# Kernel optimization log

Hardware: AMD Instinct MI355X
Metric: run time of the kernel (lower is better)

Reference implementation:

```python
import jax, jax.numpy as jnp
import numpy as np

STIM_KER_LEN = 50  # length of causal stimulus kernel
K_BASIS = 2        # number of exponential basis functions in history kernel


def setup_inputs() -> dict:
    key = jax.random.key(0)
    T, NTR = 8192, 1024
    k0, k1, k2 = jax.random.split(key, 3)
    t = jnp.arange(T, dtype=jnp.float32)                    # uniform grid, dt = 1.0
    stim = jax.random.normal(k0, (T,), jnp.float32)
    rand = jax.random.uniform(k1, (T, NTR), jnp.float32)    # per-step uniforms (torch.rand in loop)
    # learned parameters
    bias = jnp.array([-4.0], jnp.float32)                   # nn.Parameter bias
    k_stim = jax.random.normal(k2, (STIM_KER_LEN,), jnp.float32) * 0.1  # stim kernel weights
    hist_w = jnp.array([-5.0, 1.0], jnp.float32)            # exponential basis coefficients
    hist_tau = jnp.array([5.0, 20.0], jnp.float32)          # exponential basis time constants
    return dict(t=t, stim=stim, rand=rand, bias=bias, k_stim=k_stim,
                hist_w=hist_w, hist_tau=hist_tau)


def reference(t, stim, rand, bias, k_stim, hist_w, hist_tau):
    dt = t[1] - t[0]
    T = t.shape[0]
    ntr = rand.shape[1]
    # stim_kernel(stim, dt): causal convolution scaled by dt, then shift_tensor(..., 1, fill=0)
    stim_conv = jnp.convolve(stim, k_stim)[:T] * dt                       # (T,)
    stim_conv = jnp.concatenate([jnp.zeros((1,), stim.dtype), stim_conv[:-1]])
    # history kernel: ker(s) = sum_k hist_w[k] * exp(-s / hist_tau[k]), evaluated from 0
    # one step after each spike -> linear recurrence on per-basis state s (K, ntr).
    decay = jnp.exp(-dt / hist_tau)                                        # (K,)

    def step(s, inp):
        sc_j, r_j = inp                       # scalar, (ntr,)
        hist_j = jnp.sum(s, axis=0)           # (ntr,) == hist_conv[j]
        loglam_j = bias[0] + sc_j + hist_j    # (ntr,)
        p_spk = 1.0 - jnp.exp(-jnp.exp(loglam_j) * dt)
        spk_j = p_spk > r_j                   # (ntr,) bool
        s_new = decay[:, None] * s + hist_w[:, None] * spk_j.astype(s.dtype)
        return s_new, (loglam_j, spk_j)

    s0 = jnp.zeros((hist_w.shape[0], ntr), jnp.float32)
    _, (log_lam, mask_spikes) = jax.lax.scan(step, s0, (stim_conv, rand))
    return log_lam, mask_spikes
```

## Files before the change

kernel.cpp:

```cpp
#include <hip/hip_runtime.h>
#include <math.h>

#define T_LEN 8192
#define NTRIALS 1024
#define TN ((size_t)T_LEN * NTRIALS)
#define KLEN 50
#define CHUNK 64
#define NCHUNK (T_LEN / CHUNK)
#define FARW 256
#define NEARW 256
#define WARM (FARW + NEARW)
#define PF 32
#define BAND 1e-4f

__global__ __launch_bounds__(256) void prep_fused_kernel(
    const float* __restrict__ t, const float* __restrict__ stim,
    const float* __restrict__ bias, const float* __restrict__ k_stim,
    const float* __restrict__ hist_w, const float* __restrict__ hist_tau,
    const float* __restrict__ rnd, double* __restrict__ dparams,
    double* __restrict__ basc, float* __restrict__ bascf,
    float* __restrict__ thr32) {
  const int j = blockIdx.x;
  const int tid = threadIdx.x;
  const double dt = (double)t[1] - (double)t[0];

  double acc = 0.0;
  if (j > 0) {
    int n = j - 1;
    int mmax = n < (KLEN - 1) ? n : (KLEN - 1);
    for (int m = 0; m <= mmax; ++m)
      acc += (double)k_stim[m] * (double)stim[n - m];
  }
  double b64 = (double)bias[0] + (j > 0 ? dt * acc : 0.0);
  float bf = (float)b64;

  if (tid == 0) {
    basc[j] = b64;
    bascf[j] = bf;
    if (j == 0) {
      dparams[0] = exp(-dt / (double)hist_tau[0]);
      dparams[1] = exp(-dt / (double)hist_tau[1]);
      dparams[2] = (double)hist_w[0];
      dparams[3] = (double)hist_w[1];
      dparams[4] = dt;
    }
  }

  const float dtf = (float)dt;
  size_t m = (size_t)j * NTRIALS + (size_t)tid * 4;
  float4 r4 = *reinterpret_cast<const float4*>(rnd + m);
  float4 o;
  o.x = logf(-log1pf(-r4.x) / dtf) - bf;
  o.y = logf(-log1pf(-r4.y) / dtf) - bf;
  o.z = logf(-log1pf(-r4.z) / dtf) - bf;
  o.w = logf(-log1pf(-r4.w) / dtf) - bf;
  *reinterpret_cast<float4*>(thr32 + m) = o;
}

__device__ __noinline__ bool decide64(const float* __restrict__ rnd,
                                      const double* __restrict__ basc,
                                      double dt, int j, int i, double h) {
  double r = (double)rnd[(size_t)j * NTRIALS + i];
  double t = log(-log1p(-r) / dt) - basc[j];
  return h > t;
}

__global__ __launch_bounds__(64, 1) void spec_scan4_kernel(
    const float* __restrict__ thr, const float* __restrict__ rnd,
    const double* __restrict__ basc, const float* __restrict__ bascf,
    const double* __restrict__ dparams, float* __restrict__ out) {
  const int tid = threadIdx.x;
  const int tb  = blockIdx.x & 15;
  const int c   = blockIdx.x >> 4;
  const int i   = tb * 64 + tid;
  const double d0 = dparams[0], d1 = dparams[1];
  const double w0 = dparams[2], w1 = dparams[3];
  const double dt = dparams[4];
  const float d0f = (float)d0, d1f = (float)d1;
  const float w0f = (float)w0, w1f = (float)w1;

  const int jstart = c * CHUNK;
  const int nw    = jstart < WARM ? jstart : WARM;
  const int jw    = jstart - nw;
  const int nearn = nw < NEARW ? nw : NEARW;
  const int farn  = nw - nearn;
  const int j1    = jw + farn;

  const float* __restrict__ p = thr + i;
  float bufA[PF], bufB[PF];
#pragma unroll
  for (int k = 0; k < PF; ++k) bufA[k] = p[(size_t)(jw + k) * NTRIALS];
  __builtin_amdgcn_sched_barrier(0);

  float a0 = 0.0f, a1 = 0.0f;
  for (int q = 0; q < farn; q += 2 * PF) {
    const int j0 = jw + q;
#pragma unroll
    for (int k = 0; k < PF; ++k) bufB[k] = p[(size_t)(j0 + PF + k) * NTRIALS];
    __builtin_amdgcn_sched_barrier(0);
#pragma unroll
    for (int k = 0; k < PF; ++k) {
      float h = a0 + a1;
      bool s = h > bufA[k];
      a0 = fmaf(d0f, a0, s ? w0f : 0.0f);
      a1 = fmaf(d1f, a1, s ? w1f : 0.0f);
    }
    __builtin_amdgcn_sched_barrier(0);
#pragma unroll
    for (int k = 0; k < PF; ++k) bufA[k] = p[(size_t)(j0 + 2 * PF + k) * NTRIALS];
    __builtin_amdgcn_sched_barrier(0);
#pragma unroll
    for (int k = 0; k < PF; ++k) {
      float h = a0 + a1;
      bool s = h > bufB[k];
      a0 = fmaf(d0f, a0, s ? w0f : 0.0f);
      a1 = fmaf(d1f, a1, s ? w1f : 0.0f);
    }
    __builtin_amdgcn_sched_barrier(0);
  }

  double s0 = (double)a0, s1 = (double)a1;
  for (int q = 0; q < nearn; q += 2 * PF) {
    const int j0 = j1 + q;
#pragma unroll
    for (int k = 0; k < PF; ++k) bufB[k] = p[(size_t)(j0 + PF + k) * NTRIALS];
    __builtin_amdgcn_sched_barrier(0);
#pragma unroll
    for (int k = 0; k < PF; ++k) {
      double h = s0 + s1;
      float d = (float)h - bufA[k];
      bool s = d > 0.0f;
      if (__builtin_expect(fabsf(d) < BAND, 0))
        s = decide64(rnd, basc, dt, j0 + k, i, h);
      s0 = fma(d0, s0, s ? w0 : 0.0);
      s1 = fma(d1, s1, s ? w1 : 0.0);
    }
    __builtin_amdgcn_sched_barrier(0);
#pragma unroll
    for (int k = 0; k < PF; ++k) bufA[k] = p[(size_t)(j0 + 2 * PF + k) * NTRIALS];
    __builtin_amdgcn_sched_barrier(0);
#pragma unroll
    for (int k = 0; k < PF; ++k) {
      double h = s0 + s1;
      float d = (float)h - bufB[k];
      bool s = d > 0.0f;
      if (__builtin_expect(fabsf(d) < BAND, 0))
        s = decide64(rnd, basc, dt, j0 + PF + k, i, h);
      s0 = fma(d0, s0, s ? w0 : 0.0);
      s1 = fma(d1, s1, s ? w1 : 0.0);
    }
    __builtin_amdgcn_sched_barrier(0);
  }

  float* __restrict__ po_ll = out + (size_t)jstart * NTRIALS + i;
  float* __restrict__ po_mk = po_ll + TN;
#pragma unroll
  for (int k = 0; k < PF; ++k) bufB[k] = p[(size_t)(jstart + PF + k) * NTRIALS];
  __builtin_amdgcn_sched_barrier(0);
#pragma unroll
  for (int k = 0; k < PF; ++k) {
    double h = s0 + s1;
    float d = (float)h - bufA[k];
    bool s = d > 0.0f;
    if (__builtin_expect(fabsf(d) < BAND, 0))
      s = decide64(rnd, basc, dt, jstart + k, i, h);
    __builtin_nontemporal_store((float)h + bascf[jstart + k], po_ll + (size_t)k * NTRIALS);
    __builtin_nontemporal_store(s ? 1.0f : 0.0f, po_mk + (size_t)k * NTRIALS);
    s0 = fma(d0, s0, s ? w0 : 0.0);
    s1 = fma(d1, s1, s ? w1 : 0.0);
  }
  __builtin_amdgcn_sched_barrier(0);
#pragma unroll
  for (int k = 0; k < PF; ++k) {
    double h = s0 + s1;
    float d = (float)h - bufB[k];
    bool s = d > 0.0f;
    if (__builtin_expect(fabsf(d) < BAND, 0))
      s = decide64(rnd, basc, dt, jstart + PF + k, i, h);
    __builtin_nontemporal_store((float)h + bascf[jstart + PF + k], po_ll + (size_t)(PF + k) * NTRIALS);
    __builtin_nontemporal_store(s ? 1.0f : 0.0f, po_mk + (size_t)(PF + k) * NTRIALS);
    s0 = fma(d0, s0, s ? w0 : 0.0);
    s1 = fma(d1, s1, s ? w1 : 0.0);
  }
}

__global__ __launch_bounds__(64, 1) void glm_scan_inline_kernel(
    const float* __restrict__ rnd, const float* __restrict__ t,
    const float* __restrict__ stim, const float* __restrict__ bias,
    const float* __restrict__ k_stim, const float* __restrict__ hist_w,
    const float* __restrict__ hist_tau, float* __restrict__ out) {
  const int i = blockIdx.x * 64 + threadIdx.x;
  const double dt = (double)t[1] - (double)t[0];
  const double d0 = exp(-dt / (double)hist_tau[0]);
  const double d1 = exp(-dt / (double)hist_tau[1]);
  const double w0 = (double)hist_w[0], w1 = (double)hist_w[1];
  double s0 = 0.0, s1 = 0.0;
  float* __restrict__ out_ll = out;
  float* __restrict__ out_mk = out + TN;
  for (int j = 0; j < T_LEN; ++j) {
    double acc = 0.0;
    if (j > 0) {
      int n = j - 1;
      int mmax = n < (KLEN - 1) ? n : (KLEN - 1);
      for (int m = 0; m <= mmax; ++m)
        acc += (double)k_stim[m] * (double)stim[n - m];
    }
    double b = (double)bias[0] + dt * acc;
    double r = (double)rnd[(size_t)j * NTRIALS + i];
    double th = log(-log1p(-r) / dt) - b;
    double hist = s0 + s1;
    bool spk = hist > th;
    out_ll[(size_t)j * NTRIALS + i] = (float)(b + hist);
    out_mk[(size_t)j * NTRIALS + i] = spk ? 1.0f : 0.0f;
    s0 = fma(d0, s0, spk ? w0 : 0.0);
    s1 = fma(d1, s1, spk ? w1 : 0.0);
  }
}

extern "C" void kernel_launch(void* const* d_in, const int* in_sizes, int n_in,
                              void* d_out, int out_size, void* d_ws, size_t ws_size,
                              hipStream_t stream) {
  const float* t        = (const float*)d_in[0];
  const float* stim     = (const float*)d_in[1];
  const float* rnd      = (const float*)d_in[2];
  const float* bias     = (const float*)d_in[3];
  const float* k_stim   = (const float*)d_in[4];
  const float* hist_w   = (const float*)d_in[5];
  const float* hist_tau = (const float*)d_in[6];
  float* out = (float*)d_out;

  char* ws = (char*)d_ws;
  const size_t off_bascf = 64;
  const size_t off_basc  = off_bascf + (size_t)T_LEN * 4;
  const size_t off_thr   = off_basc + (size_t)T_LEN * 8;
  const size_t need_full = off_thr + TN * 4;

  double* dparams = (double*)ws;
  float*  bascf   = (float*)(ws + off_bascf);
  double* basc    = (double*)(ws + off_basc);
  float*  thr32   = (float*)(ws + off_thr);

  if (ws_size >= need_full) {
    prep_fused_kernel<<<T_LEN, 256, 0, stream>>>(
        t, stim, bias, k_stim, hist_w, hist_tau, rnd, dparams, basc, bascf, thr32);
    spec_scan4_kernel<<<NCHUNK * 16, 64, 0, stream>>>(
        thr32, rnd, basc, bascf, dparams, out);
  } else {
    glm_scan_inline_kernel<<<NTRIALS / 64, 64, 0, stream>>>(
        rnd, t, stim, bias, k_stim, hist_w, hist_tau, out);
  }
}
```

Measured before the change: 99.46 us.

## Group four chunk waves per block and run their warmup scans in lockstep

After: 116.1 us. 1.17x slower.

```diff
diff --git a/kernel.cpp b/kernel.cpp
--- a/kernel.cpp
+++ b/kernel.cpp
@@ -5,12 +5,10 @@
 #define NTRIALS 1024
 #define TN ((size_t)T_LEN * NTRIALS)
 #define KLEN 50
-#define CHUNK 64
-#define NCHUNK (T_LEN / CHUNK)
-#define FARW 256
-#define NEARW 256
-#define WARM (FARW + NEARW)
-#define PF 32
+#define MACRO 256
+#define NMACRO (T_LEN / MACRO)
+#define WX 512
+#define GP 32
 #define BAND 1e-4f
 
 __global__ __launch_bounds__(256) void prep_fused_kernel(
@@ -65,122 +63,94 @@
   return h > t;
 }
 
-__global__ __launch_bounds__(64, 1) void spec_scan4_kernel(
+__global__ __launch_bounds__(256, 1) void lockstep_scan_kernel(
     const float* __restrict__ thr, const float* __restrict__ rnd,
     const double* __restrict__ basc, const float* __restrict__ bascf,
     const double* __restrict__ dparams, float* __restrict__ out) {
-  const int tid = threadIdx.x;
-  const int tb  = blockIdx.x & 15;
-  const int c   = blockIdx.x >> 4;
-  const int i   = tb * 64 + tid;
+  const int tid  = threadIdx.x;
+  const int lane = tid & 63;
+  const int wv   = tid >> 6;
+  const int tb   = blockIdx.x & 15;
+  const int mc   = blockIdx.x >> 4;
+  const int i    = tb * 64 + lane;
+  const int J0   = mc * MACRO;
+  const int jc   = (J0 >= WX) ? (J0 - WX) : 0;
+  const int W0   = J0 + 64 * wv;
+  const int W1   = W0 + 64;
+  const int NS   = W0 - 256;
+  const int NGRP = (J0 + MACRO - jc) / GP;
+
   const double d0 = dparams[0], d1 = dparams[1];
   const double w0 = dparams[2], w1 = dparams[3];
   const double dt = dparams[4];
   const float d0f = (float)d0, d1f = (float)d1;
   const float w0f = (float)w0, w1f = (float)w1;
 
-  const int jstart = c * CHUNK;
-  const int nw    = jstart < WARM ? jstart : WARM;
-  const int jw    = jstart - nw;
-  const int nearn = nw < NEARW ? nw : NEARW;
-  const int farn  = nw - nearn;
-  const int j1    = jw + farn;
-
   const float* __restrict__ p = thr + i;
-  float bufA[PF], bufB[PF];
-#pragma unroll
-  for (int k = 0; k < PF; ++k) bufA[k] = p[(size_t)(jw + k) * NTRIALS];
-  __builtin_amdgcn_sched_barrier(0);
+  float* __restrict__ po_ll = out + i;
+  float* __restrict__ po_mk = out + TN + i;
 
   float a0 = 0.0f, a1 = 0.0f;
-  for (int q = 0; q < farn; q += 2 * PF) {
-    const int j0 = jw + q;
-#pragma unroll
-    for (int k = 0; k < PF; ++k) bufB[k] = p[(size_t)(j0 + PF + k) * NTRIALS];
-    __builtin_amdgcn_sched_barrier(0);
-#pragma unroll
-    for (int k = 0; k < PF; ++k) {
-      float h = a0 + a1;
-      bool s = h > bufA[k];
-      a0 = fmaf(d0f, a0, s ? w0f : 0.0f);
-      a1 = fmaf(d1f, a1, s ? w1f : 0.0f);
-    }
-    __builtin_amdgcn_sched_barrier(0);
-#pragma unroll
-    for (int k = 0; k < PF; ++k) bufA[k] = p[(size_t)(j0 + 2 * PF + k) * NTRIALS];
-    __builtin_amdgcn_sched_barrier(0);
-#pragma unroll
-    for (int k = 0; k < PF; ++k) {
-      float h = a0 + a1;
-      bool s = h > bufB[k];
-      a0 = fmaf(d0f, a0, s ? w0f : 0.0f);
-      a1 = fmaf(d1f, a1, s ? w1f : 0.0f);
-    }
-    __builtin_amdgcn_sched_barrier(0);
-  }
-
-  double s0 = (double)a0, s1 = (double)a1;
-  for (int q = 0; q < nearn; q += 2 * PF) {
-    const int j0 = j1 + q;
-#pragma unroll
-    for (int k = 0; k < PF; ++k) bufB[k] = p[(size_t)(j0 + PF + k) * NTRIALS];
-    __builtin_amdgcn_sched_barrier(0);
-#pragma unroll
-    for (int k = 0; k < PF; ++k) {
-      double h = s0 + s1;
-      float d = (float)h - bufA[k];
-      bool s = d > 0.0f;
-      if (__builtin_expect(fabsf(d) < BAND, 0))
-        s = decide64(rnd, basc, dt, j0 + k, i, h);
-      s0 = fma(d0, s0, s ? w0 : 0.0);
-      s1 = fma(d1, s1, s ? w1 : 0.0);
-    }
-    __builtin_amdgcn_sched_barrier(0);
-#pragma unroll
-    for (int k = 0; k < PF; ++k) bufA[k] = p[(size_t)(j0 + 2 * PF + k) * NTRIALS];
-    __builtin_amdgcn_sched_barrier(0);
-#pragma unroll
-    for (int k = 0; k < PF; ++k) {
-      double h = s0 + s1;
-      float d = (float)h - bufB[k];
-      bool s = d > 0.0f;
-      if (__builtin_expect(fabsf(d) < BAND, 0))
-        s = decide64(rnd, basc, dt, j0 + PF + k, i, h);
-      s0 = fma(d0, s0, s ? w0 : 0.0);
-      s1 = fma(d1, s1, s ? w1 : 0.0);
-    }
-    __builtin_amdgcn_sched_barrier(0);
-  }
-
-  float* __restrict__ po_ll = out + (size_t)jstart * NTRIALS + i;
-  float* __restrict__ po_mk = po_ll + TN;
-#pragma unroll
-  for (int k = 0; k < PF; ++k) bufB[k] = p[(size_t)(jstart + PF + k) * NTRIALS];
-  __builtin_amdgcn_sched_barrier(0);
-#pragma unroll
-  for (int k = 0; k < PF; ++k) {
-    double h = s0 + s1;
-    float d = (float)h - bufA[k];
-    bool s = d > 0.0f;
-    if (__builtin_expect(fabsf(d) < BAND, 0))
-      s = decide64(rnd, basc, dt, jstart + k, i, h);
-    __builtin_nontemporal_store((float)h + bascf[jstart + k], po_ll + (size_t)k * NTRIALS);
-    __builtin_nontemporal_store(s ? 1.0f : 0.0f, po_mk + (size_t)k * NTRIALS);
-    s0 = fma(d0, s0, s ? w0 : 0.0);
-    s1 = fma(d1, s1, s ? w1 : 0.0);
-  }
-  __builtin_amdgcn_sched_barrier(0);
-#pragma unroll
-  for (int k = 0; k < PF; ++k) {
-    double h = s0 + s1;
-    float d = (float)h - bufB[k];
-    bool s = d > 0.0f;
-    if (__builtin_expect(fabsf(d) < BAND, 0))
-      s = decide64(rnd, basc, dt, jstart + PF + k, i, h);
-    __builtin_nontemporal_store((float)h + bascf[jstart + PF + k], po_ll + (size_t)(PF + k) * NTRIALS);
-    __builtin_nontemporal_store(s ? 1.0f : 0.0f, po_mk + (size_t)(PF + k) * NTRIALS);
-    s0 = fma(d0, s0, s ? w0 : 0.0);
-    s1 = fma(d1, s1, s ? w1 : 0.0);
+  double s0 = 0.0, s1 = 0.0;
+  float bufA[GP], bufB[GP];
+
+  auto process = [&](int r0, float* buf) {
+    if (r0 >= W1) return;
+    if (r0 >= W0) {
+#pragma unroll
+      for (int k = 0; k < GP; ++k) {
+        double h = s0 + s1;
+        float d = (float)h - buf[k];
+        bool s = d > 0.0f;
+        if (__builtin_expect(fabsf(d) < BAND, 0))
+          s = decide64(rnd, basc, dt, r0 + k, i, h);
+        po_ll[(size_t)(r0 + k) * NTRIALS] = (float)h + bascf[r0 + k];
+        po_mk[(size_t)(r0 + k) * NTRIALS] = s ? 1.0f : 0.0f;
+        s0 = fma(d0, s0, s ? w0 : 0.0);
+        s1 = fma(d1, s1, s ? w1 : 0.0);
+      }
+    } else if (r0 >= NS) {
+      if (r0 == NS || r0 == jc) { s0 = (double)a0; s1 = (double)a1; }
+#pragma unroll
+      for (int k = 0; k < GP; ++k) {
+        double h = s0 + s1;
+        float d = (float)h - buf[k];
+        bool s = d > 0.0f;
+        if (__builtin_expect(fabsf(d) < BAND, 0))
+          s = decide64(rnd, basc, dt, r0 + k, i, h);
+        s0 = fma(d0, s0, s ? w0 : 0.0);
+        s1 = fma(d1, s1, s ? w1 : 0.0);
+      }
+    } else {
+#pragma unroll
+      for (int k = 0; k < GP; ++k) {
+        float h = a0 + a1;
+        bool s = h > buf[k];
+        a0 = fmaf(d0f, a0, s ? w0f : 0.0f);
+        a1 = fmaf(d1f, a1, s ? w1f : 0.0f);
+      }
+    }
+  };
+
+#pragma unroll
+  for (int k = 0; k < GP; ++k) bufA[k] = p[(size_t)(jc + k) * NTRIALS];
+
+  for (int g = 0; g < NGRP; g += 2) {
+    const int r0 = jc + g * GP;
+    const int r1 = r0 + GP;
+    const int r2 = r0 + 2 * GP;
+    __syncthreads();
+    if (g + 1 < NGRP && r1 < W1) {
+#pragma unroll
+      for (int k = 0; k < GP; ++k) bufB[k] = p[(size_t)(r1 + k) * NTRIALS];
+    }
+    process(r0, bufA);
+    __syncthreads();
+    if (g + 2 < NGRP && r2 < W1) {
+#pragma unroll
+      for (int k = 0; k < GP; ++k) bufA[k] = p[(size_t)(r2 + k) * NTRIALS];
+    }
+    process(r1, bufB);
   }
 }
 
@@ -243,7 +213,7 @@
   if (ws_size >= need_full) {
     prep_fused_kernel<<<T_LEN, 256, 0, stream>>>(
         t, stim, bias, k_stim, hist_w, hist_tau, rnd, dparams, basc, bascf, thr32);
-    spec_scan4_kernel<<<NCHUNK * 16, 64, 0, stream>>>(
+    lockstep_scan_kernel<<<NMACRO * 16, 256, 0, stream>>>(
         thr32, rnd, basc, bascf, dparams, out);
   } else {
     glm_scan_inline_kernel<<<NTRIALS / 64, 64, 0, stream>>>(
```
